# Performance work log

Hardware: AMD Instinct MI355X
Metric: run time of the kernel (lower is better)

The kernel has to match this reference:

```python
import jax, jax.numpy as jnp
import numpy as np


def setup_inputs() -> dict:
    key = jax.random.key(0)
    k1, k2 = jax.random.split(key)
    x = jax.random.normal(k1, (32, 112, 112, 128), dtype=jnp.float32)
    # Conv2D kernel: HWIO layout, 7x7, in=2 (mean,max), out=1
    W = jax.random.normal(k2, (7, 7, 2, 1), dtype=jnp.float32) * 0.1
    b = jnp.zeros((1,), dtype=jnp.float32)
    return {"x": x, "W": W, "b": b}


def reference(x, W, b):
    # channel statistics (NHWC, reduce over channel axis)
    mean = jnp.mean(x, axis=-1, keepdims=True)          # [B,H,W,1]
    mx = jnp.max(x, axis=-1, keepdims=True)             # [B,H,W,1]
    merged = jnp.concatenate([mean, mx], axis=-1)       # [B,H,W,2]
    # small 7x7 conv, 'same' padding, 1 output channel
    attn = jax.lax.conv_general_dilated(
        merged, W,
        window_strides=(1, 1),
        padding="SAME",
        dimension_numbers=("NHWC", "HWIO", "NHWC"),
    ) + b                                                 # [B,H,W,1]
    gate = jax.nn.sigmoid(attn)
    return x * gate                                       # broadcast multiply
```

## Files before the change

kernel.cpp:

```cpp
#include <hip/hip_runtime.h>

static constexpr int Bn = 32;
static constexpr int Hn = 112;
static constexpr int Wn = 112;
static constexpr int HALO = 3;
static constexpr int PAIRS_PER_IMG = Hn / 2;
static constexpr int NPAIR = Bn * PAIRS_PER_IMG;
static constexpr int SPIN_MAX = 150;

typedef float floatx4 __attribute__((ext_vector_type(4)));

union f2u { float2 f; unsigned long long u; };

__global__ __launch_bounds__(512) void fused_pair_kernel(const float* __restrict__ x,
                                                         const float* __restrict__ Wc,
                                                         const float* __restrict__ bias,
                                                         unsigned long long* __restrict__ stats,
                                                         int* __restrict__ flags,
                                                         float* __restrict__ out) {
    __shared__ float2 sdat[8][Wn + 2 * HALO];
    __shared__ float  glds[2][Wn];
    __shared__ float  w[98];
    __shared__ int    rowstate[8];

    const int wid  = blockIdx.x;
    const int b    = wid / PAIRS_PER_IMG;
    const int s    = wid % PAIRS_PER_IMG;
    const int r0   = 2 * s;
    const int tid  = threadIdx.x;
    const int lane = tid & 31;
    const int grp  = tid >> 5;
    const int gRow = grp >> 3;
    const int gCol = grp & 7;

    const floatx4* __restrict__ x4 = reinterpret_cast<const floatx4*>(x);
    const size_t rowbase = ((size_t)(b * Hn + r0 + gRow)) * Wn * 32;

    float xa[14], xb[14], xc[14], xd[14];
#pragma unroll
    for (int j = 0; j < 14; ++j) {
        const int c = gCol + 8 * j;
        const floatx4 v = x4[rowbase + (size_t)c * 32 + lane];
        xa[j] = v.x; xb[j] = v.y; xc[j] = v.z; xd[j] = v.w;
    }

    if (tid < 98) w[tid] = Wc[tid];
    for (int i = tid; i < 8 * (Wn + 2 * HALO); i += 512)
        ((float2*)sdat)[i] = make_float2(0.f, 0.f);
    __syncthreads();

    const size_t myStatRow = (size_t)(b * Hn + r0 + gRow) * Wn;
#pragma unroll
    for (int j = 0; j < 14; ++j) {
        const int c = gCol + 8 * j;
        float sm = xa[j] + xb[j] + xc[j] + xd[j];
        float mx = fmaxf(fmaxf(xa[j], xb[j]), fmaxf(xc[j], xd[j]));
#pragma unroll
        for (int off = 16; off >= 1; off >>= 1) {
            sm += __shfl_xor(sm, off);
            mx = fmaxf(mx, __shfl_xor(mx, off));
        }
        if (lane == 0) {
            f2u t; t.f = make_float2(sm * (1.0f / 128.0f), mx);
            sdat[3 + gRow][c + HALO] = t.f;
            __hip_atomic_store(&stats[myStatRow + c], t.u,
                               __ATOMIC_RELAXED, __HIP_MEMORY_SCOPE_AGENT);
        }
    }

#pragma unroll
    for (int j = 0; j < 14; ++j)
        asm volatile("" : "+v"(xa[j]), "+v"(xb[j]), "+v"(xc[j]), "+v"(xd[j]));

    asm volatile("s_waitcnt vmcnt(0)" ::: "memory");
    __syncthreads();
    if (tid == 0)
        __hip_atomic_store(&flags[wid], 1, __ATOMIC_RELAXED, __HIP_MEMORY_SCOPE_AGENT);

    if (tid < 8) {
        const int k = tid;
        int st;
        if (k == 3 || k == 4) st = 0;
        else {
            const int rr = r0 - HALO + k;
            if (rr < 0 || rr >= Hn) st = 2;
            else {
                const int ps = s + ((k < 3) ? ((k == 0) ? -2 : -1)
                                            : ((k == 7) ? 2 : 1));
                const int f = b * PAIRS_PER_IMG + ps;
                int it = 0, got = 0;
                do {
                    got = __hip_atomic_load(&flags[f], __ATOMIC_RELAXED,
                                            __HIP_MEMORY_SCOPE_AGENT);
                } while (!got && ++it < SPIN_MAX);
                st = got ? 1 : 3;
            }
        }
        rowstate[k] = st;
    }
    __syncthreads();

    for (int p = tid; p < 8 * Wn; p += 512) {
        const int k = p / Wn;
        const int c = p % Wn;
        if (rowstate[k] == 1) {
            const int rr = r0 - HALO + k;
            f2u t;
            t.u = __hip_atomic_load(&stats[(size_t)(b * Hn + rr) * Wn + c],
                                    __ATOMIC_RELAXED, __HIP_MEMORY_SCOPE_AGENT);
            sdat[k][c + HALO] = t.f;
        }
    }
    for (int k = 0; k < 8; ++k) {
        if (rowstate[k] != 3) continue;
        const int rr = r0 - HALO + k;
        const size_t rb = ((size_t)(b * Hn + rr)) * Wn * 32;
        for (int pc = grp; pc < Wn; pc += 16) {
            const floatx4 v = x4[rb + (size_t)pc * 32 + lane];
            float sm = v.x + v.y + v.z + v.w;
            float mx = fmaxf(fmaxf(v.x, v.y), fmaxf(v.z, v.w));
#pragma unroll
            for (int off = 16; off >= 1; off >>= 1) {
                sm += __shfl_xor(sm, off);
                mx = fmaxf(mx, __shfl_xor(mx, off));
            }
            if (lane == 0) sdat[k][pc + HALO] = make_float2(sm * (1.0f / 128.0f), mx);
        }
    }
    __syncthreads();

    if (tid < 2 * Wn) {
        const int row = tid / Wn;
        const int c   = tid % Wn;
        float acc = bias[0];
#pragma unroll
        for (int kh = 0; kh < 7; ++kh)
#pragma unroll
            for (int kw = 0; kw < 7; ++kw) {
                const float2 sv = sdat[row + kh][c + kw];
                acc = fmaf(sv.x, w[(kh * 7 + kw) * 2 + 0], acc);
                acc = fmaf(sv.y, w[(kh * 7 + kw) * 2 + 1], acc);
            }
        glds[row][c] = 1.0f / (1.0f + expf(-acc));
    }
    __syncthreads();

    floatx4* __restrict__ o4 = reinterpret_cast<floatx4*>(out);
#pragma unroll
    for (int j = 0; j < 14; ++j) {
        const int c = gCol + 8 * j;
        const float g = glds[gRow][c];
        floatx4 v;
        v.x = xa[j] * g; v.y = xb[j] * g; v.z = xc[j] * g; v.w = xd[j] * g;
        __builtin_nontemporal_store(v, &o4[rowbase + (size_t)c * 32 + lane]);
    }
}

extern "C" void kernel_launch(void* const* d_in, const int* in_sizes, int n_in,
                              void* d_out, int out_size, void* d_ws, size_t ws_size,
                              hipStream_t stream) {
    const float* x  = (const float*)d_in[0];
    const float* Wc = (const float*)d_in[1];
    const float* bb = (const float*)d_in[2];
    float* out = (float*)d_out;

    unsigned long long* stats = (unsigned long long*)d_ws;
    int* flags = (int*)((char*)d_ws + (size_t)Bn * Hn * Wn * sizeof(unsigned long long));

    hipMemsetAsync(flags, 0, NPAIR * sizeof(int), stream);
    fused_pair_kernel<<<NPAIR, 512, 0, stream>>>(x, Wc, bb, stats, flags, out);
}
```

Measured before the change: 92.81 us.

## Split work into half-row blocks with per-half halo flags

Each block now handles half of one image row (56 columns) with 256 threads, where it previously handled a pair of full rows with 512 threads. The grid grows fourfold. Halo exchange now tracks 14 neighbour half-rows, each with its own flag, and spins up to a higher limit. Smaller blocks should raise occupancy and let more blocks be resident. In exchange, each block recomputes or spins on more neighbours, so the share of halo work relative to useful work rises.

Result: faster. 90.45 us (-2.5%).

```diff
diff --git a/kernel.cpp b/kernel.cpp
--- a/kernel.cpp
+++ b/kernel.cpp
@@ -3,56 +3,55 @@
 static constexpr int Bn = 32;
 static constexpr int Hn = 112;
 static constexpr int Wn = 112;
+static constexpr int HW  = 56;
 static constexpr int HALO = 3;
-static constexpr int PAIRS_PER_IMG = Hn / 2;
-static constexpr int NPAIR = Bn * PAIRS_PER_IMG;
-static constexpr int SPIN_MAX = 150;
+static constexpr int NHALF = Bn * Hn * 2;
+static constexpr int SPIN_MAX = 200;
 
 typedef float floatx4 __attribute__((ext_vector_type(4)));
 
 union f2u { float2 f; unsigned long long u; };
 
-__global__ __launch_bounds__(512) void fused_pair_kernel(const float* __restrict__ x,
+__global__ __launch_bounds__(256) void fused_half_kernel(const float* __restrict__ x,
                                                          const float* __restrict__ Wc,
                                                          const float* __restrict__ bias,
                                                          unsigned long long* __restrict__ stats,
                                                          int* __restrict__ flags,
                                                          float* __restrict__ out) {
-    __shared__ float2 sdat[8][Wn + 2 * HALO];
-    __shared__ float  glds[2][Wn];
+    __shared__ float2 sdat[7][HW + 2 * HALO];
+    __shared__ float  glds[HW];
     __shared__ float  w[98];
-    __shared__ int    rowstate[8];
+    __shared__ int    rowstate[14];
 
-    const int wid  = blockIdx.x;
-    const int b    = wid / PAIRS_PER_IMG;
-    const int s    = wid % PAIRS_PER_IMG;
-    const int r0   = 2 * s;
-    const int tid  = threadIdx.x;
-    const int lane = tid & 31;
-    const int grp  = tid >> 5;
-    const int gRow = grp >> 3;
-    const int gCol = grp & 7;
+    const int wid   = blockIdx.x;
+    const int h     = wid & 1;
+    const int rowid = wid >> 1;
+    const int b     = rowid / Hn;
+    const int r     = rowid % Hn;
+    const int c0    = h * HW;
+    const int tid   = threadIdx.x;
+    const int lane  = tid & 31;
+    const int grp   = tid >> 5;
 
     const floatx4* __restrict__ x4 = reinterpret_cast<const floatx4*>(x);
-    const size_t rowbase = ((size_t)(b * Hn + r0 + gRow)) * Wn * 32;
+    const size_t rowbase = (size_t)rowid * Wn * 32;
 
-    float xa[14], xb[14], xc[14], xd[14];
+    float xa[7], xb[7], xc[7], xd[7];
 #pragma unroll
-    for (int j = 0; j < 14; ++j) {
-        const int c = gCol + 8 * j;
+    for (int j = 0; j < 7; ++j) {
+        const int c = c0 + grp + 8 * j;
         const floatx4 v = x4[rowbase + (size_t)c * 32 + lane];
         xa[j] = v.x; xb[j] = v.y; xc[j] = v.z; xd[j] = v.w;
     }
 
     if (tid < 98) w[tid] = Wc[tid];
-    for (int i = tid; i < 8 * (Wn + 2 * HALO); i += 512)
+    for (int i = tid; i < 7 * (HW + 2 * HALO); i += 256)
         ((float2*)sdat)[i] = make_float2(0.f, 0.f);
     __syncthreads();
 
-    const size_t myStatRow = (size_t)(b * Hn + r0 + gRow) * Wn;
 #pragma unroll
-    for (int j = 0; j < 14; ++j) {
-        const int c = gCol + 8 * j;
+    for (int j = 0; j < 7; ++j) {
+        const int c = c0 + grp + 8 * j;
         float sm = xa[j] + xb[j] + xc[j] + xd[j];
         float mx = fmaxf(fmaxf(xa[j], xb[j]), fmaxf(xc[j], xd[j]));
 #pragma unroll
@@ -62,14 +61,14 @@
         }
         if (lane == 0) {
             f2u t; t.f = make_float2(sm * (1.0f / 128.0f), mx);
-            sdat[3 + gRow][c + HALO] = t.f;
-            __hip_atomic_store(&stats[myStatRow + c], t.u,
+            sdat[HALO][c - c0 + HALO] = t.f;
+            __hip_atomic_store(&stats[(size_t)rowid * Wn + c], t.u,
                                __ATOMIC_RELAXED, __HIP_MEMORY_SCOPE_AGENT);
         }
     }
 
 #pragma unroll
-    for (int j = 0; j < 14; ++j)
+    for (int j = 0; j < 7; ++j)
         asm volatile("" : "+v"(xa[j]), "+v"(xb[j]), "+v"(xc[j]), "+v"(xd[j]));
 
     asm volatile("s_waitcnt vmcnt(0)" ::: "memory");
@@ -77,46 +76,49 @@
     if (tid == 0)
         __hip_atomic_store(&flags[wid], 1, __ATOMIC_RELAXED, __HIP_MEMORY_SCOPE_AGENT);
 
-    if (tid < 8) {
-        const int k = tid;
+    if (tid < 14) {
+        const int k  = tid >> 1;
+        const int hh = tid & 1;
         int st;
-        if (k == 3 || k == 4) st = 0;
+        const int rr = r - HALO + k;
+        if (k == HALO && hh == h) st = 0;
+        else if (rr < 0 || rr >= Hn) st = 2;
         else {
-            const int rr = r0 - HALO + k;
-            if (rr < 0 || rr >= Hn) st = 2;
-            else {
-                const int ps = s + ((k < 3) ? ((k == 0) ? -2 : -1)
-                                            : ((k == 7) ? 2 : 1));
-                const int f = b * PAIRS_PER_IMG + ps;
-                int it = 0, got = 0;
-                do {
-                    got = __hip_atomic_load(&flags[f], __ATOMIC_RELAXED,
-                                            __HIP_MEMORY_SCOPE_AGENT);
-                } while (!got && ++it < SPIN_MAX);
-                st = got ? 1 : 3;
-            }
+            const int f = ((b * Hn + rr) << 1) | hh;
+            int it = 0, got = 0;
+            do {
+                got = __hip_atomic_load(&flags[f], __ATOMIC_RELAXED,
+                                        __HIP_MEMORY_SCOPE_AGENT);
+            } while (!got && ++it < SPIN_MAX);
+            st = got ? 1 : 3;
         }
-        rowstate[k] = st;
+        rowstate[tid] = st;
     }
     __syncthreads();
 
-    for (int p = tid; p < 8 * Wn; p += 512) {
-        const int k = p / Wn;
-        const int c = p % Wn;
-        if (rowstate[k] == 1) {
-            const int rr = r0 - HALO + k;
+    for (int p = tid; p < 7 * (HW + 2 * HALO); p += 256) {
+        const int k  = p / (HW + 2 * HALO);
+        const int cc = p % (HW + 2 * HALO);
+        const int c  = c0 - HALO + cc;
+        if (c < 0 || c >= Wn) continue;
+        const int hh = c / HW;
+        if (rowstate[k * 2 + hh] == 1) {
+            const int rr = r - HALO + k;
             f2u t;
             t.u = __hip_atomic_load(&stats[(size_t)(b * Hn + rr) * Wn + c],
                                     __ATOMIC_RELAXED, __HIP_MEMORY_SCOPE_AGENT);
-            sdat[k][c + HALO] = t.f;
+            sdat[k][cc] = t.f;
         }
     }
-    for (int k = 0; k < 8; ++k) {
-        if (rowstate[k] != 3) continue;
-        const int rr = r0 - HALO + k;
-        const size_t rb = ((size_t)(b * Hn + rr)) * Wn * 32;
-        for (int pc = grp; pc < Wn; pc += 16) {
-            const floatx4 v = x4[rb + (size_t)pc * 32 + lane];
+    for (int q = 0; q < 14; ++q) {
+        if (rowstate[q] != 3) continue;
+        const int k  = q >> 1;
+        const int hh = q & 1;
+        const int rr = r - HALO + k;
+        const size_t rb = (size_t)(b * Hn + rr) * Wn * 32;
+        for (int pc = grp; pc < HW; pc += 8) {
+            const int c = hh * HW + pc;
+            const floatx4 v = x4[rb + (size_t)c * 32 + lane];
             float sm = v.x + v.y + v.z + v.w;
             float mx = fmaxf(fmaxf(v.x, v.y), fmaxf(v.z, v.w));
 #pragma unroll
@@ -124,35 +126,35 @@
                 sm += __shfl_xor(sm, off);
                 mx = fmaxf(mx, __shfl_xor(mx, off));
             }
-            if (lane == 0) sdat[k][pc + HALO] = make_float2(sm * (1.0f / 128.0f), mx);
+            const int idx = c - (c0 - HALO);
+            if (lane == 0 && idx >= 0 && idx < HW + 2 * HALO)
+                sdat[k][idx] = make_float2(sm * (1.0f / 128.0f), mx);
         }
     }
     __syncthreads();
 
-    if (tid < 2 * Wn) {
-        const int row = tid / Wn;
-        const int c   = tid % Wn;
+    if (tid < HW) {
         float acc = bias[0];
 #pragma unroll
         for (int kh = 0; kh < 7; ++kh)
 #pragma unroll
             for (int kw = 0; kw < 7; ++kw) {
-                const float2 sv = sdat[row + kh][c + kw];
+                const float2 sv = sdat[kh][tid + kw];
                 acc = fmaf(sv.x, w[(kh * 7 + kw) * 2 + 0], acc);
                 acc = fmaf(sv.y, w[(kh * 7 + kw) * 2 + 1], acc);
             }
-        glds[row][c] = 1.0f / (1.0f + expf(-acc));
+        glds[tid] = 1.0f / (1.0f + expf(-acc));
     }
     __syncthreads();
 
     floatx4* __restrict__ o4 = reinterpret_cast<floatx4*>(out);
 #pragma unroll
-    for (int j = 0; j < 14; ++j) {
-        const int c = gCol + 8 * j;
-        const float g = glds[gRow][c];
+    for (int j = 0; j < 7; ++j) {
+        const int cl = grp + 8 * j;
+        const float g = glds[cl];
         floatx4 v;
         v.x = xa[j] * g; v.y = xb[j] * g; v.z = xc[j] * g; v.w = xd[j] * g;
-        __builtin_nontemporal_store(v, &o4[rowbase + (size_t)c * 32 + lane]);
+        __builtin_nontemporal_store(v, &o4[rowbase + (size_t)(c0 + cl) * 32 + lane]);
     }
 }
 
@@ -167,6 +169,6 @@
     unsigned long long* stats = (unsigned long long*)d_ws;
     int* flags = (int*)((char*)d_ws + (size_t)Bn * Hn * Wn * sizeof(unsigned long long));
 
-    hipMemsetAsync(flags, 0, NPAIR * sizeof(int), stream);
-    fused_pair_kernel<<<NPAIR, 512, 0, stream>>>(x, Wc, bb, stats, flags, out);
+    hipMemsetAsync(flags, 0, NHALF * sizeof(int), stream);
+    fused_half_kernel<<<NHALF, 256, 0, stream>>>(x, Wc, bb, stats, flags, out);
 }
```
